# Optimization experiments

Hardware: AMD Instinct MI355X
Metric: run time of the kernel (lower is better)

## Reference

```python
import jax, jax.numpy as jnp
import numpy as np

N = 32768      # nodes
E = 524288     # edges (avg degree 16)
G = 512        # graphs in batch
F_IN = 64      # one-hot node-label dim
H = 128        # hidden_dim
C = 2          # num_classes (NCI1)
BN_EPS = 1e-3  # keras BatchNormalization default epsilon


def setup_inputs() -> dict:
    key = jax.random.key(0)
    ks = jax.random.split(key, 32)
    d = {}
    d["x"] = jax.random.normal(ks[0], (N, F_IN), jnp.float32)
    d["edge_weight"] = jax.random.uniform(ks[1], (E,), jnp.float32)
    i = 2
    din = F_IN
    for l in range(5):
        d[f"W1_{l}"] = jax.random.normal(ks[i], (din, H), jnp.float32) / np.float32(np.sqrt(din)); i += 1
        d[f"b1_{l}"] = jnp.zeros((H,), jnp.float32)
        d[f"W2_{l}"] = jax.random.normal(ks[i], (H, H), jnp.float32) / np.float32(np.sqrt(H)); i += 1
        d[f"b2_{l}"] = jnp.zeros((H,), jnp.float32)
        din = H
    for j in (1, 2, 3):  # bn1, bn2, bn3 (bn0/bn4 unused in original call())
        d[f"g{j}"] = jnp.ones((H,), jnp.float32)
        d[f"be{j}"] = jnp.zeros((H,), jnp.float32)
        d[f"m{j}"] = jnp.zeros((H,), jnp.float32)
        d[f"v{j}"] = jnp.ones((H,), jnp.float32)
    d["Wm1"] = jax.random.normal(ks[i], (5 * H, 128), jnp.float32) / np.float32(np.sqrt(5 * H)); i += 1
    d["bm1"] = jnp.zeros((128,), jnp.float32)
    d["Wm2"] = jax.random.normal(ks[i], (128, C), jnp.float32) / np.float32(np.sqrt(128.0)); i += 1
    d["bm2"] = jnp.zeros((C,), jnp.float32)
    d["edge_index"] = jax.random.randint(ks[i], (2, E), 0, N, dtype=jnp.int32); i += 1
    d["node_graph_index"] = jnp.sort(jax.random.randint(ks[i], (N,), 0, G, dtype=jnp.int32))
    return d


def reference(x, edge_weight,
              W1_0, b1_0, W2_0, b2_0,
              W1_1, b1_1, W2_1, b2_1,
              W1_2, b1_2, W2_2, b2_2,
              W1_3, b1_3, W2_3, b2_3,
              W1_4, b1_4, W2_4, b2_4,
              g1, be1, m1, v1,
              g2, be2, m2, v2,
              g3, be3, m3, v3,
              Wm1, bm1, Wm2, bm2,
              edge_index, node_graph_index):
    src, dst = edge_index[0], edge_index[1]

    def gin(h, W1, b1, W2, b2):
        # GIN with eps=0: h' = MLP(h + sum_{j in N(i)} w_ij * h_j)
        msg = h[dst] * edge_weight[:, None]              # [E, d]
        agg = jax.ops.segment_sum(msg, src, num_segments=N)
        h2 = h + agg
        return jax.nn.relu(h2 @ W1 + b1) @ W2 + b2

    def bn(h, g, be, m, v):  # inference-mode batchnorm
        return (h - m) * jax.lax.rsqrt(v + BN_EPS) * g + be

    h1 = gin(x, W1_0, b1_0, W2_0, b2_0)
    h2 = gin(bn(h1, g1, be1, m1, v1), W1_1, b1_1, W2_1, b2_1)
    h3 = gin(bn(h2, g1, be1, m1, v1), W1_2, b1_2, W2_2, b2_2)  # bn1 reused, as in source
    h4 = gin(bn(h3, g2, be2, m2, v2), W1_3, b1_3, W2_3, b2_3)
    h5 = gin(bn(h4, g3, be3, m3, v3), W1_4, b1_4, W2_4, b2_4)
    h5 = bn(h5, g3, be3, m3, v3)                                # bn3 reused, as in source

    pool = lambda h: jax.ops.segment_sum(h, node_graph_index, num_segments=G)
    hg = jnp.concatenate([pool(h1), pool(h2), pool(h3), pool(h4), pool(h5)], axis=-1)  # [G, 5H]
    # readout MLP (dropout inactive at inference)
    return jax.nn.relu(hg @ Wm1 + bm1) @ Wm2 + bm2  # [G, C]
```

## Files before the change

kernel.cpp:

```cpp
#include <hip/hip_runtime.h>
#include <hip/hip_bf16.h>

#define NN 32768
#define EE 524288
#define GG 512
#define CAP 48

typedef __bf16 bf16x8 __attribute__((ext_vector_type(8)));
typedef float  f32x4  __attribute__((ext_vector_type(4)));
typedef float  f32x2  __attribute__((ext_vector_type(2)));

#define F8_ENC 0.25f
#define F8_DEC 4.0f

static __device__ __forceinline__ float bf2f(unsigned short u) {
    union { unsigned int i; float f; } v; v.i = ((unsigned int)u) << 16; return v.f;
}
static __device__ __forceinline__ unsigned short f2bf(float f) {
    __bf16 b = (__bf16)f;
    return __builtin_bit_cast(unsigned short, b);
}
static __device__ __forceinline__ unsigned int pk2(float a, float b) {
    return (unsigned int)f2bf(a) | ((unsigned int)f2bf(b) << 16);
}
static __device__ __forceinline__ void fmaV(float* a, float w, uint4 hv) {
    a[0] += w * bf2f((unsigned short)(hv.x & 0xffff));
    a[1] += w * bf2f((unsigned short)(hv.x >> 16));
    a[2] += w * bf2f((unsigned short)(hv.y & 0xffff));
    a[3] += w * bf2f((unsigned short)(hv.y >> 16));
    a[4] += w * bf2f((unsigned short)(hv.z & 0xffff));
    a[5] += w * bf2f((unsigned short)(hv.z >> 16));
    a[6] += w * bf2f((unsigned short)(hv.w & 0xffff));
    a[7] += w * bf2f((unsigned short)(hv.w >> 16));
}
static __device__ __forceinline__ void fmaV(float* a, float w, uint2 hv) {
    a[0] += w * bf2f((unsigned short)(hv.x & 0xffff));
    a[1] += w * bf2f((unsigned short)(hv.x >> 16));
    a[2] += w * bf2f((unsigned short)(hv.y & 0xffff));
    a[3] += w * bf2f((unsigned short)(hv.y >> 16));
}
static __device__ __forceinline__ void fmaV8f8(float* a, float w, uint2 hv) {
    f32x2 p;
    p = __builtin_amdgcn_cvt_pk_f32_fp8((int)hv.x, false); a[0] += w * p[0]; a[1] += w * p[1];
    p = __builtin_amdgcn_cvt_pk_f32_fp8((int)hv.x, true);  a[2] += w * p[0]; a[3] += w * p[1];
    p = __builtin_amdgcn_cvt_pk_f32_fp8((int)hv.y, false); a[4] += w * p[0]; a[5] += w * p[1];
    p = __builtin_amdgcn_cvt_pk_f32_fp8((int)hv.y, true);  a[6] += w * p[0]; a[7] += w * p[1];
}

struct WJob { const float* in; unsigned short* out; int K; };
struct WJobs { WJob j[10]; };

__global__ __launch_bounds__(256) void build_kernel(WJobs jobs,
                                                    const int* __restrict__ src,
                                                    const int* __restrict__ dst,
                                                    const float* __restrict__ w,
                                                    int* __restrict__ cnt,
                                                    unsigned int* __restrict__ csr,
                                                    const float* __restrict__ x,
                                                    unsigned short* __restrict__ xb) {
    if (blockIdx.x < 2048) {
        int e = blockIdx.x * 256 + threadIdx.x;
        int s = src[e];
        int slot = atomicAdd(&cnt[s], 1);
        if (slot < CAP)
            csr[(size_t)s * CAP + slot] = (unsigned int)dst[e] | ((unsigned int)f2bf(w[e]) << 16);
    } else if (blockIdx.x < 2088) {
        int b = blockIdx.x - 2048;
        WJob jb = jobs.j[b >> 2];
        int quarter = b & 3;
        int per = jb.K * 128 / 4;
        for (int idx = quarter * per + threadIdx.x; idx < (quarter + 1) * per; idx += 256) {
            int k = idx >> 7, c = idx & 127;
            jb.out[c * jb.K + k] = f2bf(jb.in[idx]);
        }
    } else {
        int base = (blockIdx.x - 2088) * 4096 + threadIdx.x;
        #pragma unroll
        for (int k = 0; k < 16; ++k) {
            int idx = base + k * 256;
            xb[idx] = f2bf(x[idx]);
        }
    }
}

template<bool FIRST, bool LAST>
__global__ __launch_bounds__(256) void layer_kernel(
        const unsigned short* __restrict__ h_in,
        const unsigned char* __restrict__ h8_in,
        const int* __restrict__ cnt,
        const unsigned int* __restrict__ csr,
        const unsigned short* __restrict__ W1t,
        const float* __restrict__ b1,
        const unsigned short* __restrict__ W2t,
        const float* __restrict__ b2,
        const float* __restrict__ g, const float* __restrict__ be,
        const float* __restrict__ m, const float* __restrict__ v,
        const int* __restrict__ gidx,
        unsigned short* __restrict__ h_out,
        unsigned char* __restrict__ h8_out,
        float* __restrict__ pools, int col_off) {

    constexpr int K1 = FIRST ? 64 : 128;
    constexpr int KS1 = K1 / 32;
    constexpr int CH = FIRST ? 4 : 8;

    __shared__ unsigned int smem[2176];
    __shared__ float sscale[128], sshift[128];
    __shared__ int scnt[16];
    __shared__ int sgid[16];

    unsigned int* A1 = smem;
    unsigned int* T  = smem + 16 * 68;
    float* OUT = (float*)smem;

    int tid = threadIdx.x;
    int wave = tid >> 6, lane = tid & 63;
    int mrow = lane & 15, quad = lane >> 4;

    if (tid < 128) {
        float sc = g[tid] * rsqrtf(v[tid] + 1e-3f);
        sscale[tid] = sc;
        sshift[tid] = be[tid] - m[tid] * sc;
    } else if (tid < 144) {
        sgid[tid - 128] = gidx[blockIdx.x * 16 + (tid - 128)];
    } else if (tid < 160) {
        int d = cnt[blockIdx.x * 16 + (tid - 144)];
        scnt[tid - 144] = (d > CAP) ? CAP : d;
    }
    __syncthreads();

    {
        int i4 = lane >> 4;
        int half = (lane >> 3) & 1;
        int sub8 = lane & 7;
        int gbase = lane & 56;
        int r = wave * 4 + i4;
        int node = blockIdx.x * 16 + r;
        int deg = scnt[r];
        int md = max(max(scnt[wave * 4], scnt[wave * 4 + 1]),
                     max(scnt[wave * 4 + 2], scnt[wave * 4 + 3]));
        int mc = (md + 7) >> 3;
        size_t ebase = (size_t)node * CAP;

        unsigned int ev[6];
        #pragma unroll
        for (int c = 0; c < 6; ++c) {
            int p = c * 8 + sub8;
            unsigned int e2 = 0;
            if (p < deg) e2 = csr[ebase + p];
            ev[c] = e2;
        }

        float acc[CH];
        #pragma unroll
        for (int c = 0; c < CH; ++c) acc[c] = 0.f;

        if (FIRST) {
            const uint2* hp = (const uint2*)h_in;
            uint2 pre[4]; float wv[4];
            #pragma unroll
            for (int k = 0; k < 4; ++k) {
                unsigned int e2 = (unsigned int)__shfl((int)ev[0], gbase | k);
                wv[k] = bf2f((unsigned short)(e2 >> 16));
                pre[k] = hp[(size_t)(e2 & 0xffffu) * 16 + half * 8 + sub8];
            }
            #pragma unroll
            for (int c = 0; c < 6; ++c) {
                if (c >= mc) break;
                #pragma unroll
                for (int j = 0; j < 8; ++j) {
                    int t = c * 8 + j;
                    fmaV(acc, wv[t & 3], pre[t & 3]);
                    int tn = t + 4, cn = tn >> 3, jn = tn & 7;
                    if (cn < 6) {
                        unsigned int e2 = (unsigned int)__shfl((int)ev[cn], gbase | jn);
                        wv[t & 3] = bf2f((unsigned short)(e2 >> 16));
                        pre[t & 3] = hp[(size_t)(e2 & 0xffffu) * 16 + half * 8 + sub8];
                    }
                }
            }
            uint2 selfv = hp[(size_t)node * 16 + half * 8 + sub8];
            acc[0] += bf2f((unsigned short)(selfv.x & 0xffff));
            acc[1] += bf2f((unsigned short)(selfv.x >> 16));
            acc[2] += bf2f((unsigned short)(selfv.y & 0xffff));
            acc[3] += bf2f((unsigned short)(selfv.y >> 16));
            *(uint2*)(A1 + r * 68 + half * 16 + sub8 * 2) =
                make_uint2(pk2(acc[0], acc[1]), pk2(acc[2], acc[3]));
        } else {
            const uint2* hp8 = (const uint2*)h8_in;
            uint2 pre[4]; float wv[4];
            #pragma unroll
            for (int k = 0; k < 4; ++k) {
                unsigned int e2 = (unsigned int)__shfl((int)ev[0], gbase | k);
                wv[k] = bf2f((unsigned short)(e2 >> 16));
                pre[k] = hp8[(size_t)(e2 & 0xffffu) * 16 + half * 8 + sub8];
            }
            #pragma unroll
            for (int c = 0; c < 6; ++c) {
                if (c >= mc) break;
                #pragma unroll
                for (int j = 0; j < 8; ++j) {
                    int t = c * 8 + j;
                    fmaV8f8(acc, wv[t & 3], pre[t & 3]);
                    int tn = t + 4, cn = tn >> 3, jn = tn & 7;
                    if (cn < 6) {
                        unsigned int e2 = (unsigned int)__shfl((int)ev[cn], gbase | jn);
                        wv[t & 3] = bf2f((unsigned short)(e2 >> 16));
                        pre[t & 3] = hp8[(size_t)(e2 & 0xffffu) * 16 + half * 8 + sub8];
                    }
                }
            }
            #pragma unroll
            for (int i = 0; i < 8; ++i) acc[i] *= F8_DEC;
            const uint4* hs = (const uint4*)h_in;
            uint4 selfv = hs[(size_t)node * 16 + half * 8 + sub8];
            acc[0] += bf2f((unsigned short)(selfv.x & 0xffff));
            acc[1] += bf2f((unsigned short)(selfv.x >> 16));
            acc[2] += bf2f((unsigned short)(selfv.y & 0xffff));
            acc[3] += bf2f((unsigned short)(selfv.y >> 16));
            acc[4] += bf2f((unsigned short)(selfv.z & 0xffff));
            acc[5] += bf2f((unsigned short)(selfv.z >> 16));
            acc[6] += bf2f((unsigned short)(selfv.w & 0xffff));
            acc[7] += bf2f((unsigned short)(selfv.w >> 16));
            *(uint4*)(A1 + r * 68 + half * 32 + sub8 * 4) =
                make_uint4(pk2(acc[0], acc[1]), pk2(acc[2], acc[3]),
                           pk2(acc[4], acc[5]), pk2(acc[6], acc[7]));
        }
    }
    __syncthreads();

    const unsigned short* A1s = (const unsigned short*)A1;
    unsigned short* Ts = (unsigned short*)T;

    bf16x8 af[KS1];
    #pragma unroll
    for (int kk = 0; kk < KS1; ++kk)
        af[kk] = *(const bf16x8*)(A1s + mrow * 136 + kk * 32 + quad * 8);

    f32x4 acc1v[2];
    #pragma unroll
    for (int c = 0; c < 2; ++c) acc1v[c] = (f32x4){0.f, 0.f, 0.f, 0.f};
    #pragma unroll
    for (int c = 0; c < 2; ++c) {
        const bf16x8* Brow = (const bf16x8*)(W1t + (size_t)(wave * 32 + c * 16 + mrow) * K1);
        #pragma unroll
        for (int kk = 0; kk < KS1; ++kk)
            acc1v[c] = __builtin_amdgcn_mfma_f32_16x16x32_bf16(af[kk], Brow[kk * 4 + quad], acc1v[c], 0, 0, 0);
    }
    #pragma unroll
    for (int c = 0; c < 2; ++c) {
        int ocol = wave * 32 + c * 16 + mrow;
        float bv = b1[ocol];
        #pragma unroll
        for (int r = 0; r < 4; ++r)
            Ts[(quad * 4 + r) * 136 + ocol] = f2bf(fmaxf(acc1v[c][r] + bv, 0.f));
    }
    __syncthreads();

    bf16x8 a2f[4];
    #pragma unroll
    for (int kk = 0; kk < 4; ++kk)
        a2f[kk] = *(const bf16x8*)(Ts + mrow * 136 + kk * 32 + quad * 8);
    f32x4 acc2v[2];
    #pragma unroll
    for (int c = 0; c < 2; ++c) acc2v[c] = (f32x4){0.f, 0.f, 0.f, 0.f};
    #pragma unroll
    for (int c = 0; c < 2; ++c) {
        const bf16x8* Brow = (const bf16x8*)(W2t + (size_t)(wave * 32 + c * 16 + mrow) * 128);
        #pragma unroll
        for (int kk = 0; kk < 4; ++kk)
            acc2v[c] = __builtin_amdgcn_mfma_f32_16x16x32_bf16(a2f[kk], Brow[kk * 4 + quad], acc2v[c], 0, 0, 0);
    }
    __syncthreads();

    #pragma unroll
    for (int c = 0; c < 2; ++c) {
        int ocol = wave * 32 + c * 16 + mrow;
        float bv = b2[ocol];
        #pragma unroll
        for (int r = 0; r < 4; ++r)
            OUT[(quad * 4 + r) * 132 + ocol] = acc2v[c][r] + bv;
    }
    __syncthreads();

    if (!LAST) {
        int row = tid >> 4, q = tid & 15;
        const float* Op = OUT + row * 132 + q * 8;
        float o[8];
        #pragma unroll
        for (int i = 0; i < 8; ++i) {
            int c = q * 8 + i;
            o[i] = Op[i] * sscale[c] + sshift[c];
        }
        size_t rowbase = (size_t)(blockIdx.x * 16 + row);
        *(uint4*)(h_out + rowbase * 128 + q * 8) =
            make_uint4(pk2(o[0], o[1]), pk2(o[2], o[3]),
                       pk2(o[4], o[5]), pk2(o[6], o[7]));
        int w0 = __builtin_amdgcn_cvt_pk_fp8_f32(o[0] * F8_ENC, o[1] * F8_ENC, 0, false);
        w0 = __builtin_amdgcn_cvt_pk_fp8_f32(o[2] * F8_ENC, o[3] * F8_ENC, w0, true);
        int w1 = __builtin_amdgcn_cvt_pk_fp8_f32(o[4] * F8_ENC, o[5] * F8_ENC, 0, false);
        w1 = __builtin_amdgcn_cvt_pk_fp8_f32(o[6] * F8_ENC, o[7] * F8_ENC, w1, true);
        *(uint2*)(h8_out + rowbase * 128 + q * 8) =
            make_uint2((unsigned int)w0, (unsigned int)w1);
    }

    {
        int col = tid & 127, half = tid >> 7;
        float sc = LAST ? sscale[col] : 1.f;
        float sh = LAST ? sshift[col] : 0.f;
        float accp = 0.f;
        int cur = sgid[half * 8];
        for (int r = half * 8; r < half * 8 + 8; ++r) {
            int gi = sgid[r];
            if (gi != cur) {
                atomicAdd(&pools[(size_t)cur * 640 + col_off + col], accp);
                accp = 0.f;
                cur = gi;
            }
            float val = OUT[r * 132 + col];
            accp += LAST ? (val * sc + sh) : val;
        }
        atomicAdd(&pools[(size_t)cur * 640 + col_off + col], accp);
    }
}

__global__ __launch_bounds__(128) void readout(const float* __restrict__ pools,
                                               const float* __restrict__ Wm1,
                                               const float* __restrict__ bm1,
                                               const float* __restrict__ Wm2,
                                               const float* __restrict__ bm2,
                                               float* __restrict__ out) {
    __shared__ float row[640];
    __shared__ float partial[4];
    int gb = blockIdx.x;
    for (int k = threadIdx.x; k < 640; k += 128) row[k] = pools[(size_t)gb * 640 + k];
    __syncthreads();
    int j = threadIdx.x;
    float acc = bm1[j];
    for (int k = 0; k < 640; ++k) acc += row[k] * Wm1[(size_t)k * 128 + j];
    acc = fmaxf(acc, 0.f);
    float p0 = acc * Wm2[j * 2], p1 = acc * Wm2[j * 2 + 1];
    #pragma unroll
    for (int off = 32; off; off >>= 1) { p0 += __shfl_down(p0, off); p1 += __shfl_down(p1, off); }
    int wave = j >> 6;
    if ((j & 63) == 0) { partial[wave * 2] = p0; partial[wave * 2 + 1] = p1; }
    __syncthreads();
    if (j == 0) {
        out[gb * 2]     = bm2[0] + partial[0] + partial[2];
        out[gb * 2 + 1] = bm2[1] + partial[1] + partial[3];
    }
}

extern "C" void kernel_launch(void* const* d_in, const int* in_sizes, int n_in,
                              void* d_out, int out_size, void* d_ws, size_t ws_size,
                              hipStream_t stream) {
    const float* x  = (const float*)d_in[0];
    const float* ew = (const float*)d_in[1];
    const float *W1[5], *b1[5], *W2[5], *b2[5];
    for (int l = 0; l < 5; ++l) {
        W1[l] = (const float*)d_in[2 + 4 * l];
        b1[l] = (const float*)d_in[3 + 4 * l];
        W2[l] = (const float*)d_in[4 + 4 * l];
        b2[l] = (const float*)d_in[5 + 4 * l];
    }
    const float *bg[3], *bb[3], *bm[3], *bv[3];
    for (int j = 0; j < 3; ++j) {
        bg[j] = (const float*)d_in[22 + 4 * j];
        bb[j] = (const float*)d_in[23 + 4 * j];
        bm[j] = (const float*)d_in[24 + 4 * j];
        bv[j] = (const float*)d_in[25 + 4 * j];
    }
    const float* Wm1 = (const float*)d_in[34];
    const float* bm1 = (const float*)d_in[35];
    const float* Wm2 = (const float*)d_in[36];
    const float* bm2 = (const float*)d_in[37];
    const int* edge_index = (const int*)d_in[38];
    const int* src = edge_index;
    const int* dst = edge_index + EE;
    const int* gidx = (const int*)d_in[39];

    char* p = (char*)d_ws;
    auto alloc = [&](size_t bytes) -> void* {
        void* r = (void*)p;
        p += (bytes + 255) & ~(size_t)255;
        return r;
    };
    unsigned int* csr  = (unsigned int*)alloc((size_t)NN * CAP * 4);
    int* cnt           = (int*)alloc(NN * 4);
    unsigned short* xb = (unsigned short*)alloc((size_t)NN * 64 * 2);
    unsigned short* hA = (unsigned short*)alloc((size_t)NN * 128 * 2);
    unsigned short* hB = (unsigned short*)alloc((size_t)NN * 128 * 2);
    unsigned char* h8A = (unsigned char*)alloc((size_t)NN * 128);
    unsigned char* h8B = (unsigned char*)alloc((size_t)NN * 128);
    float* pools = (float*)alloc((size_t)GG * 640 * 4);
    unsigned short* W1t[5], *W2t[5];
    for (int l = 0; l < 5; ++l) {
        W1t[l] = (unsigned short*)alloc((size_t)128 * 128 * 2);
        W2t[l] = (unsigned short*)alloc((size_t)128 * 128 * 2);
    }

    hipMemsetAsync(cnt, 0, NN * 4, stream);
    hipMemsetAsync(pools, 0, (size_t)GG * 640 * 4, stream);

    WJobs jobs;
    for (int l = 0; l < 5; ++l) {
        jobs.j[2 * l]     = WJob{W1[l], W1t[l], (l == 0) ? 64 : 128};
        jobs.j[2 * l + 1] = WJob{W2[l], W2t[l], 128};
    }
    build_kernel<<<2048 + 40 + 512, 256, 0, stream>>>(jobs, src, dst, ew, cnt, csr, x, xb);

    const int bnsel[5] = {0, 0, 1, 2, 2};

    layer_kernel<true, false><<<NN / 16, 256, 0, stream>>>(
        xb, (const unsigned char*)nullptr, cnt, csr, W1t[0], b1[0], W2t[0], b2[0],
        bg[0], bb[0], bm[0], bv[0], gidx, hA, h8A, pools, 0);

    const unsigned short* hin = hA;
    unsigned short* hout = hB;
    const unsigned char* h8in = h8A;
    unsigned char* h8out = h8B;
    for (int l = 1; l < 5; ++l) {
        int s = bnsel[l];
        if (l < 4) {
            layer_kernel<false, false><<<NN / 16, 256, 0, stream>>>(
                hin, h8in, cnt, csr, W1t[l], b1[l], W2t[l], b2[l],
                bg[s], bb[s], bm[s], bv[s], gidx, hout, h8out, pools, l * 128);
        } else {
            layer_kernel<false, true><<<NN / 16, 256, 0, stream>>>(
                hin, h8in, cnt, csr, W1t[l], b1[l], W2t[l], b2[l],
                bg[s], bb[s], bm[s], bv[s], gidx, hout, h8out, pools, l * 128);
        }
        unsigned short* tmp = (unsigned short*)hin;
        hin = hout;
        hout = tmp;
        unsigned char* tmp8 = (unsigned char*)h8in;
        h8in = h8out;
        h8out = tmp8;
    }

    readout<<<GG, 128, 0, stream>>>(pools, Wm1, bm1, Wm2, bm2, (float*)d_out);
}
```

Before: 323.2 us.

## Fuse build, five GIN layers and readout into one persistent kernel with grid barriers

Replaces the separate build, per-layer, and readout launches with a single persistent kernel of 512 blocks. The blocks loop over node chunks and synchronise between stages with a software grid barrier built on atomics. The two memsets are merged into one. This removes kernel-launch gaps and tail effects between the seven stages. In exchange, each layer runs with 512 blocks instead of 2048, which gives less parallelism for latency hiding. The barrier also relies on all 512 blocks being co-resident on the device.

```diff
diff --git a/kernel.cpp b/kernel.cpp
--- a/kernel.cpp
+++ b/kernel.cpp
@@ -5,6 +5,7 @@
 #define EE 524288
 #define GG 512
 #define CAP 48
+#define NBLK 512
 
 typedef __bf16 bf16x8 __attribute__((ext_vector_type(8)));
 typedef float  f32x4  __attribute__((ext_vector_type(4)));
@@ -23,17 +24,7 @@
 static __device__ __forceinline__ unsigned int pk2(float a, float b) {
     return (unsigned int)f2bf(a) | ((unsigned int)f2bf(b) << 16);
 }
-static __device__ __forceinline__ void fmaV(float* a, float w, uint4 hv) {
-    a[0] += w * bf2f((unsigned short)(hv.x & 0xffff));
-    a[1] += w * bf2f((unsigned short)(hv.x >> 16));
-    a[2] += w * bf2f((unsigned short)(hv.y & 0xffff));
-    a[3] += w * bf2f((unsigned short)(hv.y >> 16));
-    a[4] += w * bf2f((unsigned short)(hv.z & 0xffff));
-    a[5] += w * bf2f((unsigned short)(hv.z >> 16));
-    a[6] += w * bf2f((unsigned short)(hv.w & 0xffff));
-    a[7] += w * bf2f((unsigned short)(hv.w >> 16));
-}
-static __device__ __forceinline__ void fmaV(float* a, float w, uint2 hv) {
+static __device__ __forceinline__ void fmaV4(float* a, float w, uint2 hv) {
     a[0] += w * bf2f((unsigned short)(hv.x & 0xffff));
     a[1] += w * bf2f((unsigned short)(hv.x >> 16));
     a[2] += w * bf2f((unsigned short)(hv.y & 0xffff));
@@ -49,66 +40,50 @@
 
 struct WJob { const float* in; unsigned short* out; int K; };
 struct WJobs { WJob j[10]; };
-
-__global__ __launch_bounds__(256) void build_kernel(WJobs jobs,
-                                                    const int* __restrict__ src,
-                                                    const int* __restrict__ dst,
-                                                    const float* __restrict__ w,
-                                                    int* __restrict__ cnt,
-                                                    unsigned int* __restrict__ csr,
-                                                    const float* __restrict__ x,
-                                                    unsigned short* __restrict__ xb) {
-    if (blockIdx.x < 2048) {
-        int e = blockIdx.x * 256 + threadIdx.x;
-        int s = src[e];
-        int slot = atomicAdd(&cnt[s], 1);
-        if (slot < CAP)
-            csr[(size_t)s * CAP + slot] = (unsigned int)dst[e] | ((unsigned int)f2bf(w[e]) << 16);
-    } else if (blockIdx.x < 2088) {
-        int b = blockIdx.x - 2048;
-        WJob jb = jobs.j[b >> 2];
-        int quarter = b & 3;
-        int per = jb.K * 128 / 4;
-        for (int idx = quarter * per + threadIdx.x; idx < (quarter + 1) * per; idx += 256) {
-            int k = idx >> 7, c = idx & 127;
-            jb.out[c * jb.K + k] = f2bf(jb.in[idx]);
-        }
-    } else {
-        int base = (blockIdx.x - 2088) * 4096 + threadIdx.x;
-        #pragma unroll
-        for (int k = 0; k < 16; ++k) {
-            int idx = base + k * 256;
-            xb[idx] = f2bf(x[idx]);
-        }
-    }
+struct LayerW {
+    const unsigned short* W1t; const float* b1;
+    const unsigned short* W2t; const float* b2;
+    const float *g, *be, *m, *v;
+};
+struct Net { LayerW lw[5]; };
+
+static __device__ __forceinline__ void gridbar(unsigned* cnt, unsigned* gen) {
+    __syncthreads();
+    if (threadIdx.x == 0) {
+        __threadfence();
+        unsigned g = __hip_atomic_load(gen, __ATOMIC_RELAXED, __HIP_MEMORY_SCOPE_AGENT);
+        unsigned arrived = __hip_atomic_fetch_add(cnt, 1u, __ATOMIC_ACQ_REL,
+                                                  __HIP_MEMORY_SCOPE_AGENT) + 1u;
+        if (arrived == (unsigned)NBLK) {
+            __hip_atomic_store(cnt, 0u, __ATOMIC_RELAXED, __HIP_MEMORY_SCOPE_AGENT);
+            __hip_atomic_fetch_add(gen, 1u, __ATOMIC_RELEASE, __HIP_MEMORY_SCOPE_AGENT);
+        } else {
+            while (__hip_atomic_load(gen, __ATOMIC_ACQUIRE, __HIP_MEMORY_SCOPE_AGENT) == g)
+                __builtin_amdgcn_s_sleep(4);
+        }
+        __threadfence();
+    }
+    __syncthreads();
 }
 
 template<bool FIRST, bool LAST>
-__global__ __launch_bounds__(256) void layer_kernel(
+static __device__ __forceinline__ void layer_chunk(
+        int chunk, unsigned int* smem, const float* sscale, const float* sshift,
+        int* scnt, int* sgid,
         const unsigned short* __restrict__ h_in,
         const unsigned char* __restrict__ h8_in,
         const int* __restrict__ cnt,
         const unsigned int* __restrict__ csr,
-        const unsigned short* __restrict__ W1t,
-        const float* __restrict__ b1,
-        const unsigned short* __restrict__ W2t,
-        const float* __restrict__ b2,
-        const float* __restrict__ g, const float* __restrict__ be,
-        const float* __restrict__ m, const float* __restrict__ v,
+        const unsigned short* __restrict__ W1t, const float* __restrict__ b1,
+        const unsigned short* __restrict__ W2t, const float* __restrict__ b2,
         const int* __restrict__ gidx,
-        unsigned short* __restrict__ h_out,
-        unsigned char* __restrict__ h8_out,
+        unsigned short* __restrict__ h_out, unsigned char* __restrict__ h8_out,
         float* __restrict__ pools, int col_off) {
 
     constexpr int K1 = FIRST ? 64 : 128;
     constexpr int KS1 = K1 / 32;
     constexpr int CH = FIRST ? 4 : 8;
 
-    __shared__ unsigned int smem[2176];
-    __shared__ float sscale[128], sshift[128];
-    __shared__ int scnt[16];
-    __shared__ int sgid[16];
-
     unsigned int* A1 = smem;
     unsigned int* T  = smem + 16 * 68;
     float* OUT = (float*)smem;
@@ -117,15 +92,11 @@
     int wave = tid >> 6, lane = tid & 63;
     int mrow = lane & 15, quad = lane >> 4;
 
-    if (tid < 128) {
-        float sc = g[tid] * rsqrtf(v[tid] + 1e-3f);
-        sscale[tid] = sc;
-        sshift[tid] = be[tid] - m[tid] * sc;
-    } else if (tid < 144) {
-        sgid[tid - 128] = gidx[blockIdx.x * 16 + (tid - 128)];
-    } else if (tid < 160) {
-        int d = cnt[blockIdx.x * 16 + (tid - 144)];
-        scnt[tid - 144] = (d > CAP) ? CAP : d;
+    if (tid < 16) {
+        sgid[tid] = gidx[chunk * 16 + tid];
+    } else if (tid < 32) {
+        int d = cnt[chunk * 16 + (tid - 16)];
+        scnt[tid - 16] = (d > CAP) ? CAP : d;
     }
     __syncthreads();
 
@@ -135,12 +106,13 @@
         int sub8 = lane & 7;
         int gbase = lane & 56;
         int r = wave * 4 + i4;
-        int node = blockIdx.x * 16 + r;
+        int node = chunk * 16 + r;
         int deg = scnt[r];
         int md = max(max(scnt[wave * 4], scnt[wave * 4 + 1]),
                      max(scnt[wave * 4 + 2], scnt[wave * 4 + 3]));
         int mc = (md + 7) >> 3;
         size_t ebase = (size_t)node * CAP;
+        int off = half * 8 + sub8;
 
         unsigned int ev[6];
         #pragma unroll
@@ -155,31 +127,34 @@
         #pragma unroll
         for (int c = 0; c < CH; ++c) acc[c] = 0.f;
 
-        if (FIRST) {
-            const uint2* hp = (const uint2*)h_in;
-            uint2 pre[4]; float wv[4];
+        const uint2* hp = FIRST ? (const uint2*)h_in : (const uint2*)h8_in;
+
+        uint2 pre[4]; float wv[4];
+        #pragma unroll
+        for (int k = 0; k < 4; ++k) {
+            unsigned int e2 = (unsigned int)__shfl((int)ev[0], gbase | k);
+            wv[k] = bf2f((unsigned short)(e2 >> 16));
+            pre[k] = hp[(size_t)(e2 & 0xffffu) * 16 + off];
+        }
+        #pragma unroll
+        for (int c = 0; c < 6; ++c) {
+            if (c >= mc) break;
             #pragma unroll
-            for (int k = 0; k < 4; ++k) {
-                unsigned int e2 = (unsigned int)__shfl((int)ev[0], gbase | k);
-                wv[k] = bf2f((unsigned short)(e2 >> 16));
-                pre[k] = hp[(size_t)(e2 & 0xffffu) * 16 + half * 8 + sub8];
-            }
-            #pragma unroll
-            for (int c = 0; c < 6; ++c) {
-                if (c >= mc) break;
-                #pragma unroll
-                for (int j = 0; j < 8; ++j) {
-                    int t = c * 8 + j;
-                    fmaV(acc, wv[t & 3], pre[t & 3]);
-                    int tn = t + 4, cn = tn >> 3, jn = tn & 7;
-                    if (cn < 6) {
-                        unsigned int e2 = (unsigned int)__shfl((int)ev[cn], gbase | jn);
-                        wv[t & 3] = bf2f((unsigned short)(e2 >> 16));
-                        pre[t & 3] = hp[(size_t)(e2 & 0xffffu) * 16 + half * 8 + sub8];
-                    }
+            for (int j = 0; j < 8; ++j) {
+                int t = c * 8 + j;
+                if constexpr (FIRST) fmaV4(acc, wv[t & 3], pre[t & 3]);
+                else                 fmaV8f8(acc, wv[t & 3], pre[t & 3]);
+                int tn = t + 4, cn = tn >> 3, jn = tn & 7;
+                if (cn < 6) {
+                    unsigned int e2 = (unsigned int)__shfl((int)ev[cn], gbase | jn);
+                    wv[t & 3] = bf2f((unsigned short)(e2 >> 16));
+                    pre[t & 3] = hp[(size_t)(e2 & 0xffffu) * 16 + off];
                 }
             }
-            uint2 selfv = hp[(size_t)node * 16 + half * 8 + sub8];
+        }
+
+        if constexpr (FIRST) {
+            uint2 selfv = ((const uint2*)h_in)[(size_t)node * 16 + off];
             acc[0] += bf2f((unsigned short)(selfv.x & 0xffff));
             acc[1] += bf2f((unsigned short)(selfv.x >> 16));
             acc[2] += bf2f((unsigned short)(selfv.y & 0xffff));
@@ -187,33 +162,9 @@
             *(uint2*)(A1 + r * 68 + half * 16 + sub8 * 2) =
                 make_uint2(pk2(acc[0], acc[1]), pk2(acc[2], acc[3]));
         } else {
-            const uint2* hp8 = (const uint2*)h8_in;
-            uint2 pre[4]; float wv[4];
-            #pragma unroll
-            for (int k = 0; k < 4; ++k) {
-                unsigned int e2 = (unsigned int)__shfl((int)ev[0], gbase | k);
-                wv[k] = bf2f((unsigned short)(e2 >> 16));
-                pre[k] = hp8[(size_t)(e2 & 0xffffu) * 16 + half * 8 + sub8];
-            }
-            #pragma unroll
-            for (int c = 0; c < 6; ++c) {
-                if (c >= mc) break;
-                #pragma unroll
-                for (int j = 0; j < 8; ++j) {
-                    int t = c * 8 + j;
-                    fmaV8f8(acc, wv[t & 3], pre[t & 3]);
-                    int tn = t + 4, cn = tn >> 3, jn = tn & 7;
-                    if (cn < 6) {
-                        unsigned int e2 = (unsigned int)__shfl((int)ev[cn], gbase | jn);
-                        wv[t & 3] = bf2f((unsigned short)(e2 >> 16));
-                        pre[t & 3] = hp8[(size_t)(e2 & 0xffffu) * 16 + half * 8 + sub8];
-                    }
-                }
-            }
             #pragma unroll
             for (int i = 0; i < 8; ++i) acc[i] *= F8_DEC;
-            const uint4* hs = (const uint4*)h_in;
-            uint4 selfv = hs[(size_t)node * 16 + half * 8 + sub8];
+            uint4 selfv = ((const uint4*)h_in)[(size_t)node * 16 + off];
             acc[0] += bf2f((unsigned short)(selfv.x & 0xffff));
             acc[1] += bf2f((unsigned short)(selfv.x >> 16));
             acc[2] += bf2f((unsigned short)(selfv.y & 0xffff));
@@ -292,7 +243,7 @@
             int c = q * 8 + i;
             o[i] = Op[i] * sscale[c] + sshift[c];
         }
-        size_t rowbase = (size_t)(blockIdx.x * 16 + row);
+        size_t rowbase = (size_t)(chunk * 16 + row);
         *(uint4*)(h_out + rowbase * 128 + q * 8) =
             make_uint4(pk2(o[0], o[1]), pk2(o[2], o[3]),
                        pk2(o[4], o[5]), pk2(o[6], o[7]));
@@ -322,32 +273,109 @@
         }
         atomicAdd(&pools[(size_t)cur * 640 + col_off + col], accp);
     }
-}
-
-__global__ __launch_bounds__(128) void readout(const float* __restrict__ pools,
-                                               const float* __restrict__ Wm1,
-                                               const float* __restrict__ bm1,
-                                               const float* __restrict__ Wm2,
-                                               const float* __restrict__ bm2,
-                                               float* __restrict__ out) {
-    __shared__ float row[640];
-    __shared__ float partial[4];
-    int gb = blockIdx.x;
-    for (int k = threadIdx.x; k < 640; k += 128) row[k] = pools[(size_t)gb * 640 + k];
-    __syncthreads();
-    int j = threadIdx.x;
-    float acc = bm1[j];
-    for (int k = 0; k < 640; ++k) acc += row[k] * Wm1[(size_t)k * 128 + j];
-    acc = fmaxf(acc, 0.f);
-    float p0 = acc * Wm2[j * 2], p1 = acc * Wm2[j * 2 + 1];
-    #pragma unroll
-    for (int off = 32; off; off >>= 1) { p0 += __shfl_down(p0, off); p1 += __shfl_down(p1, off); }
-    int wave = j >> 6;
-    if ((j & 63) == 0) { partial[wave * 2] = p0; partial[wave * 2 + 1] = p1; }
-    __syncthreads();
-    if (j == 0) {
-        out[gb * 2]     = bm2[0] + partial[0] + partial[2];
-        out[gb * 2 + 1] = bm2[1] + partial[1] + partial[3];
+    __syncthreads();
+}
+
+__global__ __launch_bounds__(256, 2) void mega_kernel(
+        WJobs jobs, Net net,
+        const float* __restrict__ x, const float* __restrict__ ew,
+        const int* __restrict__ src, const int* __restrict__ dst,
+        const int* __restrict__ gidx,
+        const float* __restrict__ Wm1, const float* __restrict__ bm1,
+        const float* __restrict__ Wm2, const float* __restrict__ bm2,
+        unsigned* __restrict__ bar,
+        int* __restrict__ cnt,
+        unsigned int* __restrict__ csr,
+        unsigned short* __restrict__ xb,
+        unsigned short* __restrict__ hA, unsigned short* __restrict__ hB,
+        unsigned char* __restrict__ h8A, unsigned char* __restrict__ h8B,
+        float* __restrict__ pools,
+        float* __restrict__ out) {
+
+    __shared__ unsigned int smem[2176];
+    __shared__ float sscale[128], sshift[128];
+    __shared__ int scnt[16];
+    __shared__ int sgid[16];
+
+    int tid = threadIdx.x, bid = blockIdx.x;
+
+    {
+        int base = bid * 256 + tid;
+        #pragma unroll
+        for (int k = 0; k < 4; ++k) {
+            int e = base + k * (NBLK * 256);
+            int s = src[e];
+            int slot = atomicAdd(&cnt[s], 1);
+            if (slot < CAP)
+                csr[(size_t)s * CAP + slot] = (unsigned int)dst[e] | ((unsigned int)f2bf(ew[e]) << 16);
+        }
+        if (bid < 40) {
+            WJob jb = jobs.j[bid >> 2];
+            int quarter = bid & 3;
+            int per = jb.K * 128 / 4;
+            for (int idx = quarter * per + tid; idx < (quarter + 1) * per; idx += 256) {
+                int k = idx >> 7, c = idx & 127;
+                jb.out[c * jb.K + k] = f2bf(jb.in[idx]);
+            }
+        }
+        int xbase = bid * 4096 + tid;
+        #pragma unroll
+        for (int k = 0; k < 16; ++k) {
+            int idx = xbase + k * 256;
+            xb[idx] = f2bf(x[idx]);
+        }
+    }
+    gridbar(bar, bar + 1);
+
+#define RUN_LAYER(L, FIRSTV, LASTV, HIN, H8IN, HOUT, H8OUT)                      \
+    {                                                                            \
+        if (tid < 128) {                                                         \
+            float sc = net.lw[L].g[tid] * rsqrtf(net.lw[L].v[tid] + 1e-3f);      \
+            sscale[tid] = sc;                                                    \
+            sshift[tid] = net.lw[L].be[tid] - net.lw[L].m[tid] * sc;             \
+        }                                                                        \
+        for (int c = bid; c < NN / 16; c += NBLK)                                \
+            layer_chunk<FIRSTV, LASTV>(c, smem, sscale, sshift, scnt, sgid,      \
+                HIN, H8IN, cnt, csr,                                             \
+                net.lw[L].W1t, net.lw[L].b1, net.lw[L].W2t, net.lw[L].b2,        \
+                gidx, HOUT, H8OUT, pools, (L) * 128);                            \
+        gridbar(bar, bar + 1);                                                   \
+    }
+
+    RUN_LAYER(0, true,  false, xb, (const unsigned char*)nullptr, hA, h8A)
+    RUN_LAYER(1, false, false, hA, h8A, hB, h8B)
+    RUN_LAYER(2, false, false, hB, h8B, hA, h8A)
+    RUN_LAYER(3, false, false, hA, h8A, hB, h8B)
+    RUN_LAYER(4, false, true,  hB, h8B, hA, h8A)
+#undef RUN_LAYER
+
+    {
+        float* row  = (float*)smem;
+        float* part = row + 704;
+        int gb = bid;
+        for (int k = tid; k < 640; k += 256) row[k] = pools[(size_t)gb * 640 + k];
+        __syncthreads();
+        int j = tid & 127, hh = tid >> 7;
+        float acc = 0.f;
+        const float* Wp = Wm1 + (size_t)(hh * 320) * 128 + j;
+        #pragma unroll 4
+        for (int k = 0; k < 320; ++k) acc += row[hh * 320 + k] * Wp[(size_t)k * 128];
+        part[tid] = acc;
+        __syncthreads();
+        if (tid < 128) {
+            float full = part[tid] + part[tid + 128] + bm1[tid];
+            full = fmaxf(full, 0.f);
+            float p0 = full * Wm2[tid * 2], p1 = full * Wm2[tid * 2 + 1];
+            #pragma unroll
+            for (int off = 32; off; off >>= 1) { p0 += __shfl_down(p0, off); p1 += __shfl_down(p1, off); }
+            int wv = tid >> 6;
+            if ((tid & 63) == 0) { part[256 + wv * 2] = p0; part[257 + wv * 2] = p1; }
+        }
+        __syncthreads();
+        if (tid == 0) {
+            out[gb * 2]     = bm2[0] + part[256] + part[258];
+            out[gb * 2 + 1] = bm2[1] + part[257] + part[259];
+        }
     }
 }
 
@@ -385,58 +413,38 @@
         p += (bytes + 255) & ~(size_t)255;
         return r;
     };
+    unsigned* bar      = (unsigned*)alloc(256);
+    int* cnt           = (int*)alloc(NN * 4);
+    float* pools       = (float*)alloc((size_t)GG * 640 * 4);
+    size_t zero_bytes  = 256 + ((size_t)NN * 4) + ((size_t)GG * 640 * 4);
+
     unsigned int* csr  = (unsigned int*)alloc((size_t)NN * CAP * 4);
-    int* cnt           = (int*)alloc(NN * 4);
     unsigned short* xb = (unsigned short*)alloc((size_t)NN * 64 * 2);
     unsigned short* hA = (unsigned short*)alloc((size_t)NN * 128 * 2);
     unsigned short* hB = (unsigned short*)alloc((size_t)NN * 128 * 2);
     unsigned char* h8A = (unsigned char*)alloc((size_t)NN * 128);
     unsigned char* h8B = (unsigned char*)alloc((size_t)NN * 128);
-    float* pools = (float*)alloc((size_t)GG * 640 * 4);
     unsigned short* W1t[5], *W2t[5];
     for (int l = 0; l < 5; ++l) {
         W1t[l] = (unsigned short*)alloc((size_t)128 * 128 * 2);
         W2t[l] = (unsigned short*)alloc((size_t)128 * 128 * 2);
     }
 
-    hipMemsetAsync(cnt, 0, NN * 4, stream);
-    hipMemsetAsync(pools, 0, (size_t)GG * 640 * 4, stream);
+    hipMemsetAsync(d_ws, 0, zero_bytes, stream);
 
     WJobs jobs;
     for (int l = 0; l < 5; ++l) {
         jobs.j[2 * l]     = WJob{W1[l], W1t[l], (l == 0) ? 64 : 128};
         jobs.j[2 * l + 1] = WJob{W2[l], W2t[l], 128};
     }
-    build_kernel<<<2048 + 40 + 512, 256, 0, stream>>>(jobs, src, dst, ew, cnt, csr, x, xb);
-
     const int bnsel[5] = {0, 0, 1, 2, 2};
-
-    layer_kernel<true, false><<<NN / 16, 256, 0, stream>>>(
-        xb, (const unsigned char*)nullptr, cnt, csr, W1t[0], b1[0], W2t[0], b2[0],
-        bg[0], bb[0], bm[0], bv[0], gidx, hA, h8A, pools, 0);
-
-    const unsigned short* hin = hA;
-    unsigned short* hout = hB;
-    const unsigned char* h8in = h8A;
-    unsigned char* h8out = h8B;
-    for (int l = 1; l < 5; ++l) {
+    Net net;
+    for (int l = 0; l < 5; ++l) {
         int s = bnsel[l];
-        if (l < 4) {
-            layer_kernel<false, false><<<NN / 16, 256, 0, stream>>>(
-                hin, h8in, cnt, csr, W1t[l], b1[l], W2t[l], b2[l],
-                bg[s], bb[s], bm[s], bv[s], gidx, hout, h8out, pools, l * 128);
-        } else {
-            layer_kernel<false, true><<<NN / 16, 256, 0, stream>>>(
-                hin, h8in, cnt, csr, W1t[l], b1[l], W2t[l], b2[l],
-                bg[s], bb[s], bm[s], bv[s], gidx, hout, h8out, pools, l * 128);
-        }
-        unsigned short* tmp = (unsigned short*)hin;
-        hin = hout;
-        hout = tmp;
-        unsigned char* tmp8 = (unsigned char*)h8in;
-        h8in = h8out;
-        h8out = tmp8;
-    }
-
-    readout<<<GG, 128, 0, stream>>>(pools, Wm1, bm1, Wm2, bm2, (float*)d_out);
-}
+        net.lw[l] = LayerW{W1t[l], b1[l], W2t[l], b2[l], bg[s], bb[s], bm[s], bv[s]};
+    }
+
+    mega_kernel<<<NBLK, 256, 0, stream>>>(
+        jobs, net, x, ew, src, dst, gidx, Wm1, bm1, Wm2, bm2,
+        bar, cnt, csr, xb, hA, hB, h8A, h8B, pools, (float*)d_out);
+}
```

Result: slower. 1.007 ms (+211.4%).

## Split fused GIN layer into separate aggregation and MLP kernels

Applied to the files above, without the earlier changes.

Each GIN layer's fused aggregate+MLP kernel becomes two kernels. A gather-only aggregation kernel with launch bounds (256, 8) writes bf16 h+agg rows to a global buffer, and the MLP kernel loads those rows into shared memory before the MFMA stages. The goal is higher occupancy for the latency-bound gather, which is no longer limited by the MLP's register and LDS use. The cost is an extra global write and read of an N×128 bf16 buffer per layer, plus five extra kernel launches.

```diff
diff --git a/kernel.cpp b/kernel.cpp
--- a/kernel.cpp
+++ b/kernel.cpp
@@ -23,17 +23,7 @@
 static __device__ __forceinline__ unsigned int pk2(float a, float b) {
     return (unsigned int)f2bf(a) | ((unsigned int)f2bf(b) << 16);
 }
-static __device__ __forceinline__ void fmaV(float* a, float w, uint4 hv) {
-    a[0] += w * bf2f((unsigned short)(hv.x & 0xffff));
-    a[1] += w * bf2f((unsigned short)(hv.x >> 16));
-    a[2] += w * bf2f((unsigned short)(hv.y & 0xffff));
-    a[3] += w * bf2f((unsigned short)(hv.y >> 16));
-    a[4] += w * bf2f((unsigned short)(hv.z & 0xffff));
-    a[5] += w * bf2f((unsigned short)(hv.z >> 16));
-    a[6] += w * bf2f((unsigned short)(hv.w & 0xffff));
-    a[7] += w * bf2f((unsigned short)(hv.w >> 16));
-}
-static __device__ __forceinline__ void fmaV(float* a, float w, uint2 hv) {
+static __device__ __forceinline__ void fmaV4(float* a, float w, uint2 hv) {
     a[0] += w * bf2f((unsigned short)(hv.x & 0xffff));
     a[1] += w * bf2f((unsigned short)(hv.x >> 16));
     a[2] += w * bf2f((unsigned short)(hv.y & 0xffff));
@@ -83,12 +73,102 @@
     }
 }
 
-template<bool FIRST, bool LAST>
-__global__ __launch_bounds__(256) void layer_kernel(
+template<bool FIRST>
+__global__ __launch_bounds__(256, 8) void agg_kernel(
         const unsigned short* __restrict__ h_in,
         const unsigned char* __restrict__ h8_in,
         const int* __restrict__ cnt,
         const unsigned int* __restrict__ csr,
+        unsigned short* __restrict__ A1g) {
+
+    constexpr int CH = FIRST ? 4 : 8;
+
+    int tid = threadIdx.x;
+    int wave = tid >> 6, lane = tid & 63;
+    int i4 = lane >> 4;
+    int half = (lane >> 3) & 1;
+    int sub8 = lane & 7;
+    int gbase = lane & 56;
+    int r = wave * 4 + i4;
+    int node = blockIdx.x * 16 + r;
+    int nb = blockIdx.x * 16 + wave * 4;
+
+    int d0 = min(cnt[nb], CAP), d1 = min(cnt[nb + 1], CAP);
+    int d2 = min(cnt[nb + 2], CAP), d3 = min(cnt[nb + 3], CAP);
+    int deg = (i4 == 0) ? d0 : (i4 == 1) ? d1 : (i4 == 2) ? d2 : d3;
+    int md = max(max(d0, d1), max(d2, d3));
+    int mc = (md + 7) >> 3;
+    size_t ebase = (size_t)node * CAP;
+    int off = half * 8 + sub8;
+
+    unsigned int ev[6];
+    #pragma unroll
+    for (int c = 0; c < 6; ++c) {
+        int p = c * 8 + sub8;
+        unsigned int e2 = 0;
+        if (p < deg) e2 = csr[ebase + p];
+        ev[c] = e2;
+    }
+
+    float acc[CH];
+    #pragma unroll
+    for (int c = 0; c < CH; ++c) acc[c] = 0.f;
+
+    const uint2* hp = FIRST ? (const uint2*)h_in : (const uint2*)h8_in;
+
+    uint2 pre[4]; float wv[4];
+    #pragma unroll
+    for (int k = 0; k < 4; ++k) {
+        unsigned int e2 = (unsigned int)__shfl((int)ev[0], gbase | k);
+        wv[k] = bf2f((unsigned short)(e2 >> 16));
+        pre[k] = hp[(size_t)(e2 & 0xffffu) * 16 + off];
+    }
+    #pragma unroll
+    for (int c = 0; c < 6; ++c) {
+        if (c >= mc) break;
+        #pragma unroll
+        for (int j = 0; j < 8; ++j) {
+            int t = c * 8 + j;
+            if constexpr (FIRST) fmaV4(acc, wv[t & 3], pre[t & 3]);
+            else                 fmaV8f8(acc, wv[t & 3], pre[t & 3]);
+            int tn = t + 4, cn = tn >> 3, jn = tn & 7;
+            if (cn < 6) {
+                unsigned int e2 = (unsigned int)__shfl((int)ev[cn], gbase | jn);
+                wv[t & 3] = bf2f((unsigned short)(e2 >> 16));
+                pre[t & 3] = hp[(size_t)(e2 & 0xffffu) * 16 + off];
+            }
+        }
+    }
+
+    if constexpr (FIRST) {
+        uint2 selfv = ((const uint2*)h_in)[(size_t)node * 16 + off];
+        acc[0] += bf2f((unsigned short)(selfv.x & 0xffff));
+        acc[1] += bf2f((unsigned short)(selfv.x >> 16));
+        acc[2] += bf2f((unsigned short)(selfv.y & 0xffff));
+        acc[3] += bf2f((unsigned short)(selfv.y >> 16));
+        *(uint2*)(A1g + (size_t)node * 64 + off * 4) =
+            make_uint2(pk2(acc[0], acc[1]), pk2(acc[2], acc[3]));
+    } else {
+        #pragma unroll
+        for (int i = 0; i < 8; ++i) acc[i] *= F8_DEC;
+        uint4 selfv = ((const uint4*)h_in)[(size_t)node * 16 + off];
+        acc[0] += bf2f((unsigned short)(selfv.x & 0xffff));
+        acc[1] += bf2f((unsigned short)(selfv.x >> 16));
+        acc[2] += bf2f((unsigned short)(selfv.y & 0xffff));
+        acc[3] += bf2f((unsigned short)(selfv.y >> 16));
+        acc[4] += bf2f((unsigned short)(selfv.z & 0xffff));
+        acc[5] += bf2f((unsigned short)(selfv.z >> 16));
+        acc[6] += bf2f((unsigned short)(selfv.w & 0xffff));
+        acc[7] += bf2f((unsigned short)(selfv.w >> 16));
+        *(uint4*)(A1g + (size_t)node * 128 + off * 8) =
+            make_uint4(pk2(acc[0], acc[1]), pk2(acc[2], acc[3]),
+                       pk2(acc[4], acc[5]), pk2(acc[6], acc[7]));
+    }
+}
+
+template<bool FIRST, bool LAST>
+__global__ __launch_bounds__(256) void mlp_kernel(
+        const unsigned short* __restrict__ A1g,
         const unsigned short* __restrict__ W1t,
         const float* __restrict__ b1,
         const unsigned short* __restrict__ W2t,
@@ -102,11 +182,9 @@
 
     constexpr int K1 = FIRST ? 64 : 128;
     constexpr int KS1 = K1 / 32;
-    constexpr int CH = FIRST ? 4 : 8;
 
     __shared__ unsigned int smem[2176];
     __shared__ float sscale[128], sshift[128];
-    __shared__ int scnt[16];
     __shared__ int sgid[16];
 
     unsigned int* A1 = smem;
@@ -123,113 +201,22 @@
         sshift[tid] = be[tid] - m[tid] * sc;
     } else if (tid < 144) {
         sgid[tid - 128] = gidx[blockIdx.x * 16 + (tid - 128)];
-    } else if (tid < 160) {
-        int d = cnt[blockIdx.x * 16 + (tid - 144)];
-        scnt[tid - 144] = (d > CAP) ? CAP : d;
-    }
-    __syncthreads();
-
-    {
-        int i4 = lane >> 4;
-        int half = (lane >> 3) & 1;
-        int sub8 = lane & 7;
-        int gbase = lane & 56;
-        int r = wave * 4 + i4;
-        int node = blockIdx.x * 16 + r;
-        int deg = scnt[r];
-        int md = max(max(scnt[wave * 4], scnt[wave * 4 + 1]),
-                     max(scnt[wave * 4 + 2], scnt[wave * 4 + 3]));
-        int mc = (md + 7) >> 3;
-        size_t ebase = (size_t)node * CAP;
-
-        unsigned int ev[6];
-        #pragma unroll
-        for (int c = 0; c < 6; ++c) {
-            int p = c * 8 + sub8;
-            unsigned int e2 = 0;
-            if (p < deg) e2 = csr[ebase + p];
-            ev[c] = e2;
-        }
-
-        float acc[CH];
-        #pragma unroll
-        for (int c = 0; c < CH; ++c) acc[c] = 0.f;
-
-        if (FIRST) {
-            const uint2* hp = (const uint2*)h_in;
-            uint2 pre[4]; float wv[4];
-            #pragma unroll
-            for (int k = 0; k < 4; ++k) {
-                unsigned int e2 = (unsigned int)__shfl((int)ev[0], gbase | k);
-                wv[k] = bf2f((unsigned short)(e2 >> 16));
-                pre[k] = hp[(size_t)(e2 & 0xffffu) * 16 + half * 8 + sub8];
-            }
-            #pragma unroll
-            for (int c = 0; c < 6; ++c) {
-                if (c >= mc) break;
-                #pragma unroll
-                for (int j = 0; j < 8; ++j) {
-                    int t = c * 8 + j;
-                    fmaV(acc, wv[t & 3], pre[t & 3]);
-                    int tn = t + 4, cn = tn >> 3, jn = tn & 7;
-                    if (cn < 6) {
-                        unsigned int e2 = (unsigned int)__shfl((int)ev[cn], gbase | jn);
-                        wv[t & 3] = bf2f((unsigned short)(e2 >> 16));
-                        pre[t & 3] = hp[(size_t)(e2 & 0xffffu) * 16 + half * 8 + sub8];
-                    }
-                }
-            }
-            uint2 selfv = hp[(size_t)node * 16 + half * 8 + sub8];
-            acc[0] += bf2f((unsigned short)(selfv.x & 0xffff));
-            acc[1] += bf2f((unsigned short)(selfv.x >> 16));
-            acc[2] += bf2f((unsigned short)(selfv.y & 0xffff));
-            acc[3] += bf2f((unsigned short)(selfv.y >> 16));
-            *(uint2*)(A1 + r * 68 + half * 16 + sub8 * 2) =
-                make_uint2(pk2(acc[0], acc[1]), pk2(acc[2], acc[3]));
-        } else {
-            const uint2* hp8 = (const uint2*)h8_in;
-            uint2 pre[4]; float wv[4];
-            #pragma unroll
-            for (int k = 0; k < 4; ++k) {
-                unsigned int e2 = (unsigned int)__shfl((int)ev[0], gbase | k);
-                wv[k] = bf2f((unsigned short)(e2 >> 16));
-                pre[k] = hp8[(size_t)(e2 & 0xffffu) * 16 + half * 8 + sub8];
-            }
-            #pragma unroll
-            for (int c = 0; c < 6; ++c) {
-                if (c >= mc) break;
-                #pragma unroll
-                for (int j = 0; j < 8; ++j) {
-                    int t = c * 8 + j;
-                    fmaV8f8(acc, wv[t & 3], pre[t & 3]);
-                    int tn = t + 4, cn = tn >> 3, jn = tn & 7;
-                    if (cn < 6) {
-                        unsigned int e2 = (unsigned int)__shfl((int)ev[cn], gbase | jn);
-                        wv[t & 3] = bf2f((unsigned short)(e2 >> 16));
-                        pre[t & 3] = hp8[(size_t)(e2 & 0xffffu) * 16 + half * 8 + sub8];
-                    }
-                }
-            }
-            #pragma unroll
-            for (int i = 0; i < 8; ++i) acc[i] *= F8_DEC;
-            const uint4* hs = (const uint4*)h_in;
-            uint4 selfv = hs[(size_t)node * 16 + half * 8 + sub8];
-            acc[0] += bf2f((unsigned short)(selfv.x & 0xffff));
-            acc[1] += bf2f((unsigned short)(selfv.x >> 16));
-            acc[2] += bf2f((unsigned short)(selfv.y & 0xffff));
-            acc[3] += bf2f((unsigned short)(selfv.y >> 16));
-            acc[4] += bf2f((unsigned short)(selfv.z & 0xffff));
-            acc[5] += bf2f((unsigned short)(selfv.z >> 16));
-            acc[6] += bf2f((unsigned short)(selfv.w & 0xffff));
-            acc[7] += bf2f((unsigned short)(selfv.w >> 16));
-            *(uint4*)(A1 + r * 68 + half * 32 + sub8 * 4) =
-                make_uint4(pk2(acc[0], acc[1]), pk2(acc[2], acc[3]),
-                           pk2(acc[4], acc[5]), pk2(acc[6], acc[7]));
-        }
-    }
-    __syncthreads();
-
-    const unsigned short* A1s = (const unsigned short*)A1;
+    }
+
+    unsigned short* A1s = (unsigned short*)A1;
+    if constexpr (FIRST) {
+        if (tid < 128) {
+            int row = tid >> 3, grp = tid & 7;
+            *(uint4*)(A1s + row * 136 + grp * 8) =
+                *(const uint4*)(A1g + (size_t)(blockIdx.x * 16 + row) * 64 + grp * 8);
+        }
+    } else {
+        int row = tid >> 4, grp = tid & 15;
+        *(uint4*)(A1s + row * 136 + grp * 8) =
+            *(const uint4*)(A1g + (size_t)(blockIdx.x * 16 + row) * 128 + grp * 8);
+    }
+    __syncthreads();
+
     unsigned short* Ts = (unsigned short*)T;
 
     bf16x8 af[KS1];
@@ -392,6 +379,7 @@
     unsigned short* hB = (unsigned short*)alloc((size_t)NN * 128 * 2);
     unsigned char* h8A = (unsigned char*)alloc((size_t)NN * 128);
     unsigned char* h8B = (unsigned char*)alloc((size_t)NN * 128);
+    unsigned short* A1g = (unsigned short*)alloc((size_t)NN * 128 * 2);
     float* pools = (float*)alloc((size_t)GG * 640 * 4);
     unsigned short* W1t[5], *W2t[5];
     for (int l = 0; l < 5; ++l) {
@@ -411,8 +399,9 @@
 
     const int bnsel[5] = {0, 0, 1, 2, 2};
 
-    layer_kernel<true, false><<<NN / 16, 256, 0, stream>>>(
-        xb, (const unsigned char*)nullptr, cnt, csr, W1t[0], b1[0], W2t[0], b2[0],
+    agg_kernel<true><<<NN / 16, 256, 0, stream>>>(xb, (const unsigned char*)nullptr, cnt, csr, A1g);
+    mlp_kernel<true, false><<<NN / 16, 256, 0, stream>>>(
+        A1g, W1t[0], b1[0], W2t[0], b2[0],
         bg[0], bb[0], bm[0], bv[0], gidx, hA, h8A, pools, 0);
 
     const unsigned short* hin = hA;
@@ -421,13 +410,14 @@
     unsigned char* h8out = h8B;
     for (int l = 1; l < 5; ++l) {
         int s = bnsel[l];
+        agg_kernel<false><<<NN / 16, 256, 0, stream>>>(hin, h8in, cnt, csr, A1g);
         if (l < 4) {
-            layer_kernel<false, false><<<NN / 16, 256, 0, stream>>>(
-                hin, h8in, cnt, csr, W1t[l], b1[l], W2t[l], b2[l],
+            mlp_kernel<false, false><<<NN / 16, 256, 0, stream>>>(
+                A1g, W1t[l], b1[l], W2t[l], b2[l],
                 bg[s], bb[s], bm[s], bv[s], gidx, hout, h8out, pools, l * 128);
         } else {
-            layer_kernel<false, true><<<NN / 16, 256, 0, stream>>>(
-                hin, h8in, cnt, csr, W1t[l], b1[l], W2t[l], b2[l],
+            mlp_kernel<false, true><<<NN / 16, 256, 0, stream>>>(
+                A1g, W1t[l], b1[l], W2t[l], b2[l],
                 bg[s], bb[s], bm[s], bv[s], gidx, hout, h8out, pools, l * 128);
         }
         unsigned short* tmp = (unsigned short*)hin;
```

Result: slower. 342.9 us (+6.1%).
